# Kernel optimization log

Measured on AMD Instinct MI355X. Metric: run time of the kernel, lower is better.

The kernel has to match this reference:

```python
import jax, jax.numpy as jnp
import numpy as np

B, S, D = 2, 2048, 1024
H = 16
HD = D // H  # 64

def setup_inputs() -> dict:
    key = jax.random.key(0)
    ks = jax.random.split(key, 6)
    s = 1.0 / np.sqrt(D)
    return {
        "x": jax.random.normal(ks[0], (B, S, D), dtype=jnp.float32),
        "Wq": jax.random.normal(ks[1], (D, D), dtype=jnp.float32) * s,
        "Wk": jax.random.normal(ks[2], (D, D), dtype=jnp.float32) * s,
        "Wv": jax.random.normal(ks[3], (D, D), dtype=jnp.float32) * s,
        "Wo": jax.random.normal(ks[4], (D, D), dtype=jnp.float32) * s,
        "bo": jax.random.normal(ks[5], (D,), dtype=jnp.float32) * 0.01,
    }

def reference(x, Wq, Wk, Wv, Wo, bo):
    b, n, _ = x.shape
    # qkv projections (nn.Linear: x @ W^T, no bias for qkv)
    q = (x @ Wq.T).reshape(b, n, H, HD).transpose(0, 2, 1, 3)  # [B,H,S,hd]
    k = (x @ Wk.T).reshape(b, n, H, HD).transpose(0, 2, 1, 3)
    v = (x @ Wv.T).reshape(b, n, H, HD).transpose(0, 2, 1, 3)
    scores = jnp.einsum('bhqd,bhkd->bhqk', q, k)  # [B,H,S,S]
    causal = jnp.triu(jnp.ones((n, n), dtype=bool), k=1)
    scores = jnp.where(causal, -jnp.inf, scores)
    attn = jax.nn.softmax(scores / np.sqrt(HD), axis=-1)
    ctx = jnp.einsum('bhqk,bhkd->bhqd', attn, v)  # [B,H,S,hd]
    ctx = ctx.transpose(0, 2, 1, 3).reshape(b, n, D)
    return ctx @ Wo.T + bo
```

## Files before the change

kernel.cpp:

```cpp
#include <hip/hip_runtime.h>
#include <hip/hip_bf16.h>

typedef __hip_bfloat16 bf16;
typedef short v8s __attribute__((ext_vector_type(8)));
typedef float v4f __attribute__((ext_vector_type(4)));

#define S_ 2048
#define D_ 1024
#define H_ 16
#define HD_ 64

#define EXP2F(x) __builtin_amdgcn_exp2f(x)
#define NEG_BIG (-1.0e30f)
#define C2 0.1803368801111244f

#define GLDS16(g, l) __builtin_amdgcn_global_load_lds(                        \
    (const __attribute__((address_space(1))) unsigned int*)(g),               \
    (__attribute__((address_space(3))) unsigned int*)(l), 16, 0, 0)

static __device__ __forceinline__ unsigned short bf16_bits(bf16 h) {
    union { bf16 h; unsigned short u; } c; c.h = h; return c.u;
}

static __device__ __forceinline__ v8s pack_bf16x8(const float4 a, const float4 b) {
    union { v8s v; unsigned short u[8]; } r;
    r.u[0] = bf16_bits(__float2bfloat16(a.x));
    r.u[1] = bf16_bits(__float2bfloat16(a.y));
    r.u[2] = bf16_bits(__float2bfloat16(a.z));
    r.u[3] = bf16_bits(__float2bfloat16(a.w));
    r.u[4] = bf16_bits(__float2bfloat16(b.x));
    r.u[5] = bf16_bits(__float2bfloat16(b.y));
    r.u[6] = bf16_bits(__float2bfloat16(b.z));
    r.u[7] = bf16_bits(__float2bfloat16(b.w));
    return r.v;
}

__global__ __launch_bounds__(256)
void cvt_bf16(const float* __restrict__ x,  const float* __restrict__ wq,
              const float* __restrict__ wk, const float* __restrict__ wv,
              const float* __restrict__ wo,
              bf16* __restrict__ xb,  bf16* __restrict__ wqb,
              bf16* __restrict__ wkb, bf16* __restrict__ wvb,
              bf16* __restrict__ wob)
{
    const int seg = blockIdx.y;
    const float* src; bf16* dst; int n;
    switch (seg) {
        case 0: src = x;  dst = xb;  n = 4096 * 1024; break;
        case 1: src = wq; dst = wqb; n = 1024 * 1024; break;
        case 2: src = wk; dst = wkb; n = 1024 * 1024; break;
        case 3: src = wv; dst = wvb; n = 1024 * 1024; break;
        default:src = wo; dst = wob; n = 1024 * 1024; break;
    }
    const int idx = (blockIdx.x * 256 + threadIdx.x) * 8;
    if (idx >= n) return;
    *(v8s*)&dst[idx] = pack_bf16x8(*(const float4*)&src[idx],
                                   *(const float4*)&src[idx + 4]);
}

__global__ __launch_bounds__(256)
void gemm_qkv_f(const bf16* __restrict__ xb, const bf16* __restrict__ wqb,
                const bf16* __restrict__ wkb, const bf16* __restrict__ wvb,
                bf16* __restrict__ qd, bf16* __restrict__ kd, bf16* __restrict__ vtd)
{
    const int mode = blockIdx.z;
    const bf16* __restrict__ W = (mode == 0) ? wqb : (mode == 1) ? wkb : wvb;
    const int m0 = blockIdx.x * 128;
    const int n0 = blockIdx.y * 128;
    __shared__ bf16 As[128 * 32];
    __shared__ bf16 Bs[128 * 32];
    const int t    = threadIdx.x;
    const int lane = t & 63, w = t >> 6;
    const int wr = w >> 1, wc = w & 1;
    const int l15 = lane & 15, quad = lane >> 4;
    const int r16 = lane >> 2, c8 = (lane & 3) * 8;
    v4f acc[4][4] = {};

    const bf16* ga = &xb[(m0 + w*16 + r16) * 1024 + c8];
    const bf16* gb = &W [(n0 + w*16 + r16) * 1024 + c8];
    bf16* la0 = &As[w * 16 * 32];
    bf16* la1 = &As[(64 + w * 16) * 32];
    bf16* lb0 = &Bs[w * 16 * 32];
    bf16* lb1 = &Bs[(64 + w * 16) * 32];

    for (int k0 = 0; k0 < 1024; k0 += 32) {
        __syncthreads();
        GLDS16(ga + k0,             la0);
        GLDS16(ga + k0 + 64 * 1024, la1);
        GLDS16(gb + k0,             lb0);
        GLDS16(gb + k0 + 64 * 1024, lb1);
        __syncthreads();
        v8s a[4], b[4];
#pragma unroll
        for (int mt = 0; mt < 4; mt++) a[mt] = *(const v8s*)&As[(wr*64 + mt*16 + l15)*32 + quad*8];
#pragma unroll
        for (int nt = 0; nt < 4; nt++) b[nt] = *(const v8s*)&Bs[(wc*64 + nt*16 + l15)*32 + quad*8];
#pragma unroll
        for (int mt = 0; mt < 4; mt++)
#pragma unroll
            for (int nt = 0; nt < 4; nt++)
                acc[mt][nt] = __builtin_amdgcn_mfma_f32_16x16x32_bf16(a[mt], b[nt], acc[mt][nt], 0, 0, 0);
    }

    const float qscale = (mode == 0) ? C2 : 1.0f;
#pragma unroll
    for (int mt = 0; mt < 4; mt++) {
        const int mb = m0 + wr*64 + mt*16 + quad*4;
        const int b_ = mb >> 11, s = mb & 2047;
#pragma unroll
        for (int nt = 0; nt < 4; nt++) {
            const int n = n0 + wc*64 + nt*16 + l15;
            const int h = n >> 6, d = n & 63;
            if (mode == 2) {
                unsigned int lo = (unsigned int)bf16_bits(__float2bfloat16(acc[mt][nt][0]))
                                | ((unsigned int)bf16_bits(__float2bfloat16(acc[mt][nt][1])) << 16);
                unsigned int hi = (unsigned int)bf16_bits(__float2bfloat16(acc[mt][nt][2]))
                                | ((unsigned int)bf16_bits(__float2bfloat16(acc[mt][nt][3])) << 16);
                uint2 pv; pv.x = lo; pv.y = hi;
                *(uint2*)&vtd[((b_*H_ + h)*HD_ + d)*S_ + s] = pv;
            } else {
                bf16* __restrict__ dst = (mode == 0) ? qd : kd;
#pragma unroll
                for (int r = 0; r < 4; r++)
                    dst[((b_*H_ + h)*S_ + (s + r))*HD_ + d] = __float2bfloat16(acc[mt][nt][r] * qscale);
            }
        }
    }
}

__global__ __launch_bounds__(256)
void gemm_out_f(const bf16* __restrict__ ctx, const bf16* __restrict__ wob,
                const float* __restrict__ bo, float* __restrict__ out)
{
    const int m0 = blockIdx.x * 128;
    const int n0 = blockIdx.y * 128;
    __shared__ bf16 As[128 * 32];
    __shared__ bf16 Bs[128 * 32];
    const int t    = threadIdx.x;
    const int lane = t & 63, w = t >> 6;
    const int wr = w >> 1, wc = w & 1;
    const int l15 = lane & 15, quad = lane >> 4;
    const int r16 = lane >> 2, c8 = (lane & 3) * 8;
    v4f acc[4][4] = {};

    const bf16* ga = &ctx[(m0 + w*16 + r16) * 1024 + c8];
    const bf16* gb = &wob[(n0 + w*16 + r16) * 1024 + c8];
    bf16* la0 = &As[w * 16 * 32];
    bf16* la1 = &As[(64 + w * 16) * 32];
    bf16* lb0 = &Bs[w * 16 * 32];
    bf16* lb1 = &Bs[(64 + w * 16) * 32];

    for (int k0 = 0; k0 < 1024; k0 += 32) {
        __syncthreads();
        GLDS16(ga + k0,             la0);
        GLDS16(ga + k0 + 64 * 1024, la1);
        GLDS16(gb + k0,             lb0);
        GLDS16(gb + k0 + 64 * 1024, lb1);
        __syncthreads();
        v8s a[4], b[4];
#pragma unroll
        for (int mt = 0; mt < 4; mt++) a[mt] = *(const v8s*)&As[(wr*64 + mt*16 + l15)*32 + quad*8];
#pragma unroll
        for (int nt = 0; nt < 4; nt++) b[nt] = *(const v8s*)&Bs[(wc*64 + nt*16 + l15)*32 + quad*8];
#pragma unroll
        for (int mt = 0; mt < 4; mt++)
#pragma unroll
            for (int nt = 0; nt < 4; nt++)
                acc[mt][nt] = __builtin_amdgcn_mfma_f32_16x16x32_bf16(a[mt], b[nt], acc[mt][nt], 0, 0, 0);
    }

#pragma unroll
    for (int mt = 0; mt < 4; mt++) {
        const int mb = m0 + wr*64 + mt*16 + quad*4;
#pragma unroll
        for (int nt = 0; nt < 4; nt++) {
            const int n = n0 + wc*64 + nt*16 + l15;
            const float bias = bo[n];
#pragma unroll
            for (int r = 0; r < 4; r++)
                out[(mb + r)*1024 + n] = acc[mt][nt][r] + bias;
        }
    }
}

__global__ __launch_bounds__(256)
void gemm_qkv(const float* __restrict__ x, const float* __restrict__ Wq,
              const float* __restrict__ Wk, const float* __restrict__ Wv,
              bf16* __restrict__ qd, bf16* __restrict__ kd, bf16* __restrict__ vtd)
{
    const int mode = blockIdx.z;
    const float* __restrict__ W = (mode == 0) ? Wq : (mode == 1) ? Wk : Wv;
    const int m0 = blockIdx.x * 128;
    const int n0 = blockIdx.y * 128;
    __shared__ bf16 As[128 * 40];
    __shared__ bf16 Bs[128 * 40];
    const int t    = threadIdx.x;
    const int lane = t & 63, w = t >> 6;
    const int wr = w >> 1, wc = w & 1;
    const int l15 = lane & 15, quad = lane >> 4;
    const int srow = t >> 2, scol = (t & 3) * 8;
    v4f acc[4][4] = {};

    for (int k0 = 0; k0 < 1024; k0 += 32) {
        __syncthreads();
        {
            const float* pa = &x[(m0 + srow) * 1024 + k0 + scol];
            *(v8s*)&As[srow*40 + scol] = pack_bf16x8(*(const float4*)pa, *(const float4*)(pa + 4));
            const float* pa2 = pa + 64 * 1024;
            *(v8s*)&As[(srow+64)*40 + scol] = pack_bf16x8(*(const float4*)pa2, *(const float4*)(pa2 + 4));
            const float* pb = &W[(n0 + srow) * 1024 + k0 + scol];
            *(v8s*)&Bs[srow*40 + scol] = pack_bf16x8(*(const float4*)pb, *(const float4*)(pb + 4));
            const float* pb2 = pb + 64 * 1024;
            *(v8s*)&Bs[(srow+64)*40 + scol] = pack_bf16x8(*(const float4*)pb2, *(const float4*)(pb2 + 4));
        }
        __syncthreads();
        v8s a[4], b[4];
#pragma unroll
        for (int mt = 0; mt < 4; mt++) a[mt] = *(const v8s*)&As[(wr*64 + mt*16 + l15)*40 + quad*8];
#pragma unroll
        for (int nt = 0; nt < 4; nt++) b[nt] = *(const v8s*)&Bs[(wc*64 + nt*16 + l15)*40 + quad*8];
#pragma unroll
        for (int mt = 0; mt < 4; mt++)
#pragma unroll
            for (int nt = 0; nt < 4; nt++)
                acc[mt][nt] = __builtin_amdgcn_mfma_f32_16x16x32_bf16(a[mt], b[nt], acc[mt][nt], 0, 0, 0);
    }

    const float qscale = (mode == 0) ? C2 : 1.0f;
#pragma unroll
    for (int mt = 0; mt < 4; mt++) {
        const int mb = m0 + wr*64 + mt*16 + quad*4;
        const int b_ = mb >> 11, s = mb & 2047;
#pragma unroll
        for (int nt = 0; nt < 4; nt++) {
            const int n = n0 + wc*64 + nt*16 + l15;
            const int h = n >> 6, d = n & 63;
            if (mode == 2) {
                unsigned int lo = (unsigned int)bf16_bits(__float2bfloat16(acc[mt][nt][0]))
                                | ((unsigned int)bf16_bits(__float2bfloat16(acc[mt][nt][1])) << 16);
                unsigned int hi = (unsigned int)bf16_bits(__float2bfloat16(acc[mt][nt][2]))
                                | ((unsigned int)bf16_bits(__float2bfloat16(acc[mt][nt][3])) << 16);
                uint2 pv; pv.x = lo; pv.y = hi;
                *(uint2*)&vtd[((b_*H_ + h)*HD_ + d)*S_ + s] = pv;
            } else {
                bf16* __restrict__ dst = (mode == 0) ? qd : kd;
#pragma unroll
                for (int r = 0; r < 4; r++)
                    dst[((b_*H_ + h)*S_ + (s + r))*HD_ + d] = __float2bfloat16(acc[mt][nt][r] * qscale);
            }
        }
    }
}

__global__ __launch_bounds__(256)
void gemm_out(const bf16* __restrict__ ctx, const float* __restrict__ Wo,
              const float* __restrict__ bo, float* __restrict__ out)
{
    const int m0 = blockIdx.x * 128;
    const int n0 = blockIdx.y * 128;
    __shared__ bf16 As[128 * 40];
    __shared__ bf16 Bs[128 * 40];
    const int t    = threadIdx.x;
    const int lane = t & 63, w = t >> 6;
    const int wr = w >> 1, wc = w & 1;
    const int l15 = lane & 15, quad = lane >> 4;
    const int srow = t >> 2, scol = (t & 3) * 8;
    v4f acc[4][4] = {};

    for (int k0 = 0; k0 < 1024; k0 += 32) {
        __syncthreads();
        {
            *(v8s*)&As[srow*40 + scol]      = *(const v8s*)&ctx[(m0+srow)*1024 + k0 + scol];
            *(v8s*)&As[(srow+64)*40 + scol] = *(const v8s*)&ctx[(m0+srow+64)*1024 + k0 + scol];
            const float* pb = &Wo[(n0 + srow) * 1024 + k0 + scol];
            *(v8s*)&Bs[srow*40 + scol] = pack_bf16x8(*(const float4*)pb, *(const float4*)(pb + 4));
            const float* pb2 = pb + 64 * 1024;
            *(v8s*)&Bs[(srow+64)*40 + scol] = pack_bf16x8(*(const float4*)pb2, *(const float4*)(pb2 + 4));
        }
        __syncthreads();
        v8s a[4], b[4];
#pragma unroll
        for (int mt = 0; mt < 4; mt++) a[mt] = *(const v8s*)&As[(wr*64 + mt*16 + l15)*40 + quad*8];
#pragma unroll
        for (int nt = 0; nt < 4; nt++) b[nt] = *(const v8s*)&Bs[(wc*64 + nt*16 + l15)*40 + quad*8];
#pragma unroll
        for (int mt = 0; mt < 4; mt++)
#pragma unroll
            for (int nt = 0; nt < 4; nt++)
                acc[mt][nt] = __builtin_amdgcn_mfma_f32_16x16x32_bf16(a[mt], b[nt], acc[mt][nt], 0, 0, 0);
    }

#pragma unroll
    for (int mt = 0; mt < 4; mt++) {
        const int mb = m0 + wr*64 + mt*16 + quad*4;
#pragma unroll
        for (int nt = 0; nt < 4; nt++) {
            const int n = n0 + wc*64 + nt*16 + l15;
            const float bias = bo[n];
#pragma unroll
            for (int r = 0; r < 4; r++)
                out[(mb + r)*1024 + n] = acc[mt][nt][r] + bias;
        }
    }
}

__global__ __launch_bounds__(256)
void flash_attn(const bf16* __restrict__ qd, const bf16* __restrict__ kd,
                const bf16* __restrict__ vtd, bf16* __restrict__ ctx)
{
    const int bh = blockIdx.x;
    const int qb = 15 - blockIdx.y;
    const int t = threadIdx.x;
    const int lane = t & 63, w = t >> 6;
    const int l15 = lane & 15, quad = lane >> 4;
    const int q0 = qb * 128;
    const int nT = 2 * qb + 2;

    __shared__ bf16 Ks[2][64 * 72];
    __shared__ bf16 Vs[2][64 * 72];
    __shared__ bf16 Pl[4][16 * 72];

    const int mrow0 = q0 + w * 16;
    const int mrow1 = q0 + 64 + w * 16;

    v8s qf[2][2];
#pragma unroll
    for (int mt = 0; mt < 2; mt++) {
        const bf16* qb_ = qd + (bh*S_ + (mt ? mrow1 : mrow0) + l15) * HD_;
        qf[mt][0] = *(const v8s*)(qb_ + quad*8);
        qf[mt][1] = *(const v8s*)(qb_ + 32 + quad*8);
    }

    v4f o[2][4] = {};
    float ps[2][4] = {};

    const int rowlo = t >> 3, col8 = (t & 7) * 8;
    const bf16* kp = kd  + (bh*S_ + rowlo)*HD_ + col8;
    const bf16* vp = vtd + (bh*HD_ + rowlo)*S_ + col8;

    v8s pk0 = *(const v8s*)(kp);
    v8s pk1 = *(const v8s*)(kp + 32*HD_);
    v8s pv0 = *(const v8s*)(vp);
    v8s pv1 = *(const v8s*)(vp + 32*S_);

    for (int it = 0; it < nT; ++it) {
        const int c0 = it * 64;
        bf16* Kb = &Ks[it & 1][0];
        bf16* Vb = &Vs[it & 1][0];
        *(v8s*)&Kb[rowlo*72 + col8]      = pk0;
        *(v8s*)&Kb[(rowlo+32)*72 + col8] = pk1;
        *(v8s*)&Vb[rowlo*72 + col8]      = pv0;
        *(v8s*)&Vb[(rowlo+32)*72 + col8] = pv1;
        __syncthreads();
        kp += 64 * HD_;
        vp += 64;
        pk0 = *(const v8s*)(kp);
        pk1 = *(const v8s*)(kp + 32*HD_);
        pv0 = *(const v8s*)(vp);
        pv1 = *(const v8s*)(vp + 32*S_);

        if (c0 <= mrow1 + 15) {
            v8s kf[4][2];
#pragma unroll
            for (int kt = 0; kt < 4; kt++) {
                kf[kt][0] = *(const v8s*)&Kb[(kt*16 + l15)*72 + quad*8];
                kf[kt][1] = *(const v8s*)&Kb[(kt*16 + l15)*72 + 32 + quad*8];
            }
            v8s vf[4][2];
#pragma unroll
            for (int dt = 0; dt < 4; dt++) {
                vf[dt][0] = *(const v8s*)&Vb[(dt*16 + l15)*72 + quad*8];
                vf[dt][1] = *(const v8s*)&Vb[(dt*16 + l15)*72 + 32 + quad*8];
            }

#pragma unroll
            for (int mt = 0; mt < 2; mt++) {
                const int mr = mt ? mrow1 : mrow0;
                if (c0 > mr + 15) continue;
                v4f sc[4] = {};
#pragma unroll
                for (int kt = 0; kt < 4; kt++) {
                    sc[kt] = __builtin_amdgcn_mfma_f32_16x16x32_bf16(qf[mt][0], kf[kt][0], sc[kt], 0, 0, 0);
                    sc[kt] = __builtin_amdgcn_mfma_f32_16x16x32_bf16(qf[mt][1], kf[kt][1], sc[kt], 0, 0, 0);
                }
                const bool full = (c0 + 63 <= mr);
#pragma unroll
                for (int r = 0; r < 4; r++) {
                    const int qg = mr + quad*4 + r;
#pragma unroll
                    for (int kt = 0; kt < 4; kt++) {
                        float s = sc[kt][r];
                        if (!full) {
                            const int kg = c0 + kt*16 + l15;
                            s = (kg <= qg) ? s : NEG_BIG;
                        }
                        const float p = EXP2F(s);
                        sc[kt][r] = p;
                        ps[mt][r] += p;
                    }
                }
                bf16* pw = &Pl[w][0];
#pragma unroll
                for (int kt = 0; kt < 4; kt++)
#pragma unroll
                    for (int r = 0; r < 4; r++)
                        pw[(quad*4 + r)*72 + kt*16 + l15] = __float2bfloat16(sc[kt][r]);
                v8s pf0 = *(const v8s*)&pw[l15*72 + quad*8];
                v8s pf1 = *(const v8s*)&pw[l15*72 + 32 + quad*8];
#pragma unroll
                for (int dt = 0; dt < 4; dt++) {
                    o[mt][dt] = __builtin_amdgcn_mfma_f32_16x16x32_bf16(pf0, vf[dt][0], o[mt][dt], 0, 0, 0);
                    o[mt][dt] = __builtin_amdgcn_mfma_f32_16x16x32_bf16(pf1, vf[dt][1], o[mt][dt], 0, 0, 0);
                }
            }
        }
    }

    const int b_ = bh >> 4, h = bh & 15;
#pragma unroll
    for (int mt = 0; mt < 2; mt++) {
        const int mr = mt ? mrow1 : mrow0;
#pragma unroll
        for (int r = 0; r < 4; r++) {
            float l = ps[mt][r];
#pragma unroll
            for (int off = 1; off < 16; off <<= 1) l += __shfl_xor(l, off);
            const float linv = 1.0f / l;
            const int qg = mr + quad*4 + r;
#pragma unroll
            for (int dt = 0; dt < 4; dt++)
                ctx[(b_*S_ + qg)*D_ + h*HD_ + dt*16 + l15] = __float2bfloat16(o[mt][dt][r] * linv);
        }
    }
}

extern "C" void kernel_launch(void* const* d_in, const int* in_sizes, int n_in,
                              void* d_out, int out_size, void* d_ws, size_t ws_size,
                              hipStream_t stream) {
    const float* x  = (const float*)d_in[0];
    const float* Wq = (const float*)d_in[1];
    const float* Wk = (const float*)d_in[2];
    const float* Wv = (const float*)d_in[3];
    const float* Wo = (const float*)d_in[4];
    const float* bo = (const float*)d_in[5];
    float* out = (float*)d_out;

    const size_t SEG = (size_t)2 * H_ * S_ * HD_;
    bf16* qd  = (bf16*)d_ws;
    bf16* kd  = qd  + SEG;
    bf16* vtd = kd  + SEG;
    bf16* xc  = vtd + SEG;
    bf16* wqb = xc + SEG;
    bf16* wkb = wqb + 1024 * 1024;
    bf16* wvb = wkb + 1024 * 1024;
    bf16* wvv = wvb;
    bf16* wob = wvb + 1024 * 1024;
    (void)wvv;

    const size_t need_fast = (4 * SEG + 4 * 1024 * 1024) * sizeof(bf16);

    if (ws_size >= need_fast) {
        cvt_bf16<<<dim3(2048, 5), 256, 0, stream>>>(x, Wq, Wk, Wv, Wo,
                                                    xc, wqb, wkb, wvb, wob);
        gemm_qkv_f<<<dim3(32, 8, 3), 256, 0, stream>>>(xc, wqb, wkb, wvb, qd, kd, vtd);
        flash_attn<<<dim3(32, 16), 256, 0, stream>>>(qd, kd, vtd, xc);
        gemm_out_f<<<dim3(32, 8), 256, 0, stream>>>(xc, wob, bo, out);
    } else {
        gemm_qkv<<<dim3(32, 8, 3), 256, 0, stream>>>(x, Wq, Wk, Wv, qd, kd, vtd);
        flash_attn<<<dim3(32, 16), 256, 0, stream>>>(qd, kd, vtd, xc);
        gemm_out<<<dim3(32, 8), 256, 0, stream>>>(xc, Wo, bo, out);
    }
}
```

Baseline: 209.3 us.

## Pair causal query blocks per workgroup and load K fragments directly from global

Flash attention now launches 512-thread workgroups that each handle a mirrored pair of query blocks (p and 15-p), so every workgroup does the same amount of causal work and the grid is halved. K tiles are no longer staged through LDS. Each wave loads its K MFMA fragments straight from global memory and prefetches the next tile in registers. Only V still goes through double-buffered LDS, now filled with one 16-byte load per thread. The goal is to remove causal load imbalance and LDS traffic for K, at the cost of redundant K global loads across waves and higher register pressure.

After: 208.4 us. No clear change (-0.4%).

```diff
diff --git a/kernel.cpp b/kernel.cpp
--- a/kernel.cpp
+++ b/kernel.cpp
@@ -304,24 +304,24 @@
     }
 }
 
-__global__ __launch_bounds__(256)
+__global__ __launch_bounds__(512)
 void flash_attn(const bf16* __restrict__ qd, const bf16* __restrict__ kd,
                 const bf16* __restrict__ vtd, bf16* __restrict__ ctx)
 {
     const int bh = blockIdx.x;
-    const int qb = 15 - blockIdx.y;
+    const int p  = blockIdx.y;
     const int t = threadIdx.x;
     const int lane = t & 63, w = t >> 6;
     const int l15 = lane & 15, quad = lane >> 4;
-    const int q0 = qb * 128;
-    const int nT = 2 * qb + 2;
-
-    __shared__ bf16 Ks[2][64 * 72];
+    const int side = w >> 2, wl = w & 3;
+    const int q0 = (side ? (15 - p) : p) * 128;
+    const int nT = 32 - 2 * p;
+
     __shared__ bf16 Vs[2][64 * 72];
-    __shared__ bf16 Pl[4][16 * 72];
-
-    const int mrow0 = q0 + w * 16;
-    const int mrow1 = q0 + 64 + w * 16;
+    __shared__ bf16 Pl[8][16 * 72];
+
+    const int mrow0 = q0 + wl * 16;
+    const int mrow1 = q0 + 64 + wl * 16;
 
     v8s qf[2][2];
 #pragma unroll
@@ -335,37 +335,39 @@
     float ps[2][4] = {};
 
     const int rowlo = t >> 3, col8 = (t & 7) * 8;
-    const bf16* kp = kd  + (bh*S_ + rowlo)*HD_ + col8;
     const bf16* vp = vtd + (bh*HD_ + rowlo)*S_ + col8;
-
-    v8s pk0 = *(const v8s*)(kp);
-    v8s pk1 = *(const v8s*)(kp + 32*HD_);
-    v8s pv0 = *(const v8s*)(vp);
-    v8s pv1 = *(const v8s*)(vp + 32*S_);
+    v8s pv = *(const v8s*)vp;
+
+    const bf16* kbase = kd + (size_t)bh * S_ * HD_;
+    v8s kf[4][2];
+#pragma unroll
+    for (int kt = 0; kt < 4; kt++) {
+        const bf16* kp_ = kbase + (kt*16 + l15)*HD_ + quad*8;
+        kf[kt][0] = *(const v8s*)kp_;
+        kf[kt][1] = *(const v8s*)(kp_ + 32);
+    }
 
     for (int it = 0; it < nT; ++it) {
         const int c0 = it * 64;
-        bf16* Kb = &Ks[it & 1][0];
         bf16* Vb = &Vs[it & 1][0];
-        *(v8s*)&Kb[rowlo*72 + col8]      = pk0;
-        *(v8s*)&Kb[(rowlo+32)*72 + col8] = pk1;
-        *(v8s*)&Vb[rowlo*72 + col8]      = pv0;
-        *(v8s*)&Vb[(rowlo+32)*72 + col8] = pv1;
-        __syncthreads();
-        kp += 64 * HD_;
+        *(v8s*)&Vb[rowlo*72 + col8] = pv;
+        __syncthreads();
         vp += 64;
-        pk0 = *(const v8s*)(kp);
-        pk1 = *(const v8s*)(kp + 32*HD_);
-        pv0 = *(const v8s*)(vp);
-        pv1 = *(const v8s*)(vp + 32*S_);
-
-        if (c0 <= mrow1 + 15) {
-            v8s kf[4][2];
+        pv = *(const v8s*)vp;
+
+        const bool act  = (c0      <= mrow1 + 15);
+        const bool nact = (c0 + 64 <= mrow1 + 15);
+        v8s nkf[4][2];
+        if (nact) {
 #pragma unroll
             for (int kt = 0; kt < 4; kt++) {
-                kf[kt][0] = *(const v8s*)&Kb[(kt*16 + l15)*72 + quad*8];
-                kf[kt][1] = *(const v8s*)&Kb[(kt*16 + l15)*72 + 32 + quad*8];
+                const bf16* kp_ = kbase + (c0 + 64 + kt*16 + l15)*HD_ + quad*8;
+                nkf[kt][0] = *(const v8s*)kp_;
+                nkf[kt][1] = *(const v8s*)(kp_ + 32);
             }
+        }
+
+        if (act) {
             v8s vf[4][2];
 #pragma unroll
             for (int dt = 0; dt < 4; dt++) {
@@ -394,9 +396,9 @@
                             const int kg = c0 + kt*16 + l15;
                             s = (kg <= qg) ? s : NEG_BIG;
                         }
-                        const float p = EXP2F(s);
-                        sc[kt][r] = p;
-                        ps[mt][r] += p;
+                        const float pp = EXP2F(s);
+                        sc[kt][r] = pp;
+                        ps[mt][r] += pp;
                     }
                 }
                 bf16* pw = &Pl[w][0];
@@ -413,6 +415,10 @@
                     o[mt][dt] = __builtin_amdgcn_mfma_f32_16x16x32_bf16(pf1, vf[dt][1], o[mt][dt], 0, 0, 0);
                 }
             }
+        }
+        if (nact) {
+#pragma unroll
+            for (int kt = 0; kt < 4; kt++) { kf[kt][0] = nkf[kt][0]; kf[kt][1] = nkf[kt][1]; }
         }
     }
 
@@ -453,9 +459,7 @@
     bf16* wqb = xc + SEG;
     bf16* wkb = wqb + 1024 * 1024;
     bf16* wvb = wkb + 1024 * 1024;
-    bf16* wvv = wvb;
     bf16* wob = wvb + 1024 * 1024;
-    (void)wvv;
 
     const size_t need_fast = (4 * SEG + 4 * 1024 * 1024) * sizeof(bf16);
 
@@ -463,11 +467,11 @@
         cvt_bf16<<<dim3(2048, 5), 256, 0, stream>>>(x, Wq, Wk, Wv, Wo,
                                                     xc, wqb, wkb, wvb, wob);
         gemm_qkv_f<<<dim3(32, 8, 3), 256, 0, stream>>>(xc, wqb, wkb, wvb, qd, kd, vtd);
-        flash_attn<<<dim3(32, 16), 256, 0, stream>>>(qd, kd, vtd, xc);
+        flash_attn<<<dim3(32, 8), 512, 0, stream>>>(qd, kd, vtd, xc);
         gemm_out_f<<<dim3(32, 8), 256, 0, stream>>>(xc, wob, bo, out);
     } else {
         gemm_qkv<<<dim3(32, 8, 3), 256, 0, stream>>>(x, Wq, Wk, Wv, qd, kd, vtd);
-        flash_attn<<<dim3(32, 16), 256, 0, stream>>>(qd, kd, vtd, xc);
+        flash_attn<<<dim3(32, 8), 512, 0, stream>>>(qd, kd, vtd, xc);
         gemm_out<<<dim3(32, 8), 256, 0, stream>>>(xc, Wo, bo, out);
     }
 }
```

## Restructure flash attention: 64-row tiles, K from registers, shuffle-built P operand

Applied to the files above, without the earlier changes.

Each attention block now covers 64 query rows (one 16-row tile per wave), and the grid doubles to 32x32 blocks. K fragments are loaded straight from global memory into registers and prefetched one tile ahead, so the K shared-memory buffer and its staging go away. Scores are computed transposed (K·Q). The softmax probabilities are packed with v_cvt_pk_bf16_f32 and rearranged into the MFMA A operand through cross-lane shuffles instead of a round trip through shared memory. V moves to an XOR-swizzled 64-wide LDS layout; the trade-offs are more blocks and more per-block K global loads in exchange for less LDS traffic and finer causal load balance.

After: 223.0 us. 1.07x slower.

```diff
diff --git a/kernel.cpp b/kernel.cpp
--- a/kernel.cpp
+++ b/kernel.cpp
@@ -17,6 +17,9 @@
 #define GLDS16(g, l) __builtin_amdgcn_global_load_lds(                        \
     (const __attribute__((address_space(1))) unsigned int*)(g),               \
     (__attribute__((address_space(3))) unsigned int*)(l), 16, 0, 0)
+
+#define CVT_PK(d, lo, hi) \
+    asm("v_cvt_pk_bf16_f32 %0, %1, %2" : "=v"(d) : "v"(lo), "v"(hi))
 
 static __device__ __forceinline__ unsigned short bf16_bits(bf16 h) {
     union { bf16 h; unsigned short u; } c; c.h = h; return c.u;
@@ -309,128 +312,146 @@
                 const bf16* __restrict__ vtd, bf16* __restrict__ ctx)
 {
     const int bh = blockIdx.x;
-    const int qb = 15 - blockIdx.y;
+    const int s  = 31 - (int)blockIdx.y;
     const int t = threadIdx.x;
     const int lane = t & 63, w = t >> 6;
     const int l15 = lane & 15, quad = lane >> 4;
-    const int q0 = qb * 128;
-    const int nT = 2 * qb + 2;
-
-    __shared__ bf16 Ks[2][64 * 72];
-    __shared__ bf16 Vs[2][64 * 72];
-    __shared__ bf16 Pl[4][16 * 72];
-
-    const int mrow0 = q0 + w * 16;
-    const int mrow1 = q0 + 64 + w * 16;
-
-    v8s qf[2][2];
-#pragma unroll
-    for (int mt = 0; mt < 2; mt++) {
-        const bf16* qb_ = qd + (bh*S_ + (mt ? mrow1 : mrow0) + l15) * HD_;
-        qf[mt][0] = *(const v8s*)(qb_ + quad*8);
-        qf[mt][1] = *(const v8s*)(qb_ + 32 + quad*8);
-    }
-
-    v4f o[2][4] = {};
-    float ps[2][4] = {};
-
-    const int rowlo = t >> 3, col8 = (t & 7) * 8;
-    const bf16* kp = kd  + (bh*S_ + rowlo)*HD_ + col8;
-    const bf16* vp = vtd + (bh*HD_ + rowlo)*S_ + col8;
-
-    v8s pk0 = *(const v8s*)(kp);
-    v8s pk1 = *(const v8s*)(kp + 32*HD_);
-    v8s pv0 = *(const v8s*)(vp);
-    v8s pv1 = *(const v8s*)(vp + 32*S_);
+    const int q0 = s * 64 + w * 16;
+    const int nT = s + 1;
+
+    __shared__ bf16 Vs[2][64 * 64];
+
+    const bf16* qp = qd + ((size_t)bh * S_ + q0 + l15) * HD_ + quad * 8;
+    const v8s qf0 = *(const v8s*)qp;
+    const v8s qf1 = *(const v8s*)(qp + 32);
+
+    v4f o[4] = {};
+    float ps = 0.0f;
+
+    const int vrow = t >> 2, vc = (t & 3) * 16;
+    const int wsw = (vrow & 7) << 3;
+    const int vidx0 = (vrow * 64 + vc) ^ wsw;
+    const int vidx1 = (vrow * 64 + vc + 8) ^ wsw;
+    const bf16* vp = vtd + ((size_t)bh * HD_ + vrow) * S_ + vc;
+    v8s pv0 = *(const v8s*)vp;
+    v8s pv1 = *(const v8s*)(vp + 8);
+
+    const bf16* kq = kd + ((size_t)bh * S_ + l15) * HD_ + quad * 8;
+    v8s kf[4][2];
+#pragma unroll
+    for (int kt = 0; kt < 4; kt++) {
+        kf[kt][0] = *(const v8s*)(kq + (kt * 16) * HD_);
+        kf[kt][1] = *(const v8s*)(kq + (kt * 16) * HD_ + 32);
+    }
+
+    const int rsw = (l15 & 7) << 3;
 
     for (int it = 0; it < nT; ++it) {
         const int c0 = it * 64;
-        bf16* Kb = &Ks[it & 1][0];
         bf16* Vb = &Vs[it & 1][0];
-        *(v8s*)&Kb[rowlo*72 + col8]      = pk0;
-        *(v8s*)&Kb[(rowlo+32)*72 + col8] = pk1;
-        *(v8s*)&Vb[rowlo*72 + col8]      = pv0;
-        *(v8s*)&Vb[(rowlo+32)*72 + col8] = pv1;
-        __syncthreads();
-        kp += 64 * HD_;
+        *(v8s*)&Vb[vidx0] = pv0;
+        *(v8s*)&Vb[vidx1] = pv1;
+        __syncthreads();
         vp += 64;
-        pk0 = *(const v8s*)(kp);
-        pk1 = *(const v8s*)(kp + 32*HD_);
-        pv0 = *(const v8s*)(vp);
-        pv1 = *(const v8s*)(vp + 32*S_);
-
-        if (c0 <= mrow1 + 15) {
-            v8s kf[4][2];
+        pv0 = *(const v8s*)vp;
+        pv1 = *(const v8s*)(vp + 8);
+
+        v8s vf[4][2];
+#pragma unroll
+        for (int dt = 0; dt < 4; dt++) {
+            const int rowd = dt * 16 + l15;
+            vf[dt][0] = *(const v8s*)&Vb[(rowd * 64 + quad * 8) ^ rsw];
+            vf[dt][1] = *(const v8s*)&Vb[(rowd * 64 + 32 + quad * 8) ^ rsw];
+        }
+
+        v4f sc[4];
+#pragma unroll
+        for (int kt = 0; kt < 4; kt++) {
+            v4f z = {};
+            z      = __builtin_amdgcn_mfma_f32_16x16x32_bf16(kf[kt][0], qf0, z, 0, 0, 0);
+            sc[kt] = __builtin_amdgcn_mfma_f32_16x16x32_bf16(kf[kt][1], qf1, sc[kt] = z, 0, 0, 0);
+        }
+
+        if (it + 1 < nT) {
+            const bf16* kn = kq + (size_t)(c0 + 64) * HD_;
 #pragma unroll
             for (int kt = 0; kt < 4; kt++) {
-                kf[kt][0] = *(const v8s*)&Kb[(kt*16 + l15)*72 + quad*8];
-                kf[kt][1] = *(const v8s*)&Kb[(kt*16 + l15)*72 + 32 + quad*8];
+                kf[kt][0] = *(const v8s*)(kn + (kt * 16) * HD_);
+                kf[kt][1] = *(const v8s*)(kn + (kt * 16) * HD_ + 32);
             }
-            v8s vf[4][2];
-#pragma unroll
-            for (int dt = 0; dt < 4; dt++) {
-                vf[dt][0] = *(const v8s*)&Vb[(dt*16 + l15)*72 + quad*8];
-                vf[dt][1] = *(const v8s*)&Vb[(dt*16 + l15)*72 + 32 + quad*8];
-            }
-
-#pragma unroll
-            for (int mt = 0; mt < 2; mt++) {
-                const int mr = mt ? mrow1 : mrow0;
-                if (c0 > mr + 15) continue;
-                v4f sc[4] = {};
-#pragma unroll
-                for (int kt = 0; kt < 4; kt++) {
-                    sc[kt] = __builtin_amdgcn_mfma_f32_16x16x32_bf16(qf[mt][0], kf[kt][0], sc[kt], 0, 0, 0);
-                    sc[kt] = __builtin_amdgcn_mfma_f32_16x16x32_bf16(qf[mt][1], kf[kt][1], sc[kt], 0, 0, 0);
+        }
+
+        if (c0 + 63 <= q0) {
+#pragma unroll
+            for (int kt = 0; kt < 4; kt++)
+#pragma unroll
+                for (int r = 0; r < 4; r++) {
+                    const float p = EXP2F(sc[kt][r]);
+                    sc[kt][r] = p; ps += p;
                 }
-                const bool full = (c0 + 63 <= mr);
+        } else {
+            const int kb = c0 - q0 - l15 + quad * 4;
+#pragma unroll
+            for (int kt = 0; kt < 4; kt++)
 #pragma unroll
                 for (int r = 0; r < 4; r++) {
-                    const int qg = mr + quad*4 + r;
-#pragma unroll
-                    for (int kt = 0; kt < 4; kt++) {
-                        float s = sc[kt][r];
-                        if (!full) {
-                            const int kg = c0 + kt*16 + l15;
-                            s = (kg <= qg) ? s : NEG_BIG;
-                        }
-                        const float p = EXP2F(s);
-                        sc[kt][r] = p;
-                        ps[mt][r] += p;
-                    }
+                    const float sv = (kb + kt * 16 + r <= 0) ? sc[kt][r] : NEG_BIG;
+                    const float p = EXP2F(sv);
+                    sc[kt][r] = p; ps += p;
                 }
-                bf16* pw = &Pl[w][0];
-#pragma unroll
-                for (int kt = 0; kt < 4; kt++)
-#pragma unroll
-                    for (int r = 0; r < 4; r++)
-                        pw[(quad*4 + r)*72 + kt*16 + l15] = __float2bfloat16(sc[kt][r]);
-                v8s pf0 = *(const v8s*)&pw[l15*72 + quad*8];
-                v8s pf1 = *(const v8s*)&pw[l15*72 + 32 + quad*8];
-#pragma unroll
-                for (int dt = 0; dt < 4; dt++) {
-                    o[mt][dt] = __builtin_amdgcn_mfma_f32_16x16x32_bf16(pf0, vf[dt][0], o[mt][dt], 0, 0, 0);
-                    o[mt][dt] = __builtin_amdgcn_mfma_f32_16x16x32_bf16(pf1, vf[dt][1], o[mt][dt], 0, 0, 0);
-                }
-            }
-        }
-    }
-
+        }
+
+        unsigned W[4][2];
+#pragma unroll
+        for (int kt = 0; kt < 4; kt++) {
+            CVT_PK(W[kt][0], sc[kt][0], sc[kt][1]);
+            CVT_PK(W[kt][1], sc[kt][2], sc[kt][3]);
+        }
+        const bool qhi = quad >= 2;
+        unsigned X0 = qhi ? W[0][0] : W[1][0];
+        unsigned X1 = qhi ? W[0][1] : W[1][1];
+        unsigned X2 = qhi ? W[2][0] : W[3][0];
+        unsigned X3 = qhi ? W[2][1] : W[3][1];
+        const unsigned A0 = __shfl_xor(X0, 32);
+        const unsigned A1 = __shfl_xor(X1, 32);
+        const unsigned A2 = __shfl_xor(X2, 32);
+        const unsigned A3 = __shfl_xor(X3, 32);
+        unsigned Z0 = (quad == 1) ? W[0][0] : (quad == 2) ? W[1][0] : A0;
+        unsigned Z1 = (quad == 1) ? W[0][1] : (quad == 2) ? W[1][1] : A1;
+        unsigned Z2 = (quad == 1) ? W[2][0] : (quad == 2) ? W[3][0] : A2;
+        unsigned Z3 = (quad == 1) ? W[2][1] : (quad == 2) ? W[3][1] : A3;
+        const unsigned B0 = __shfl_xor(Z0, 16);
+        const unsigned B1 = __shfl_xor(Z1, 16);
+        const unsigned B2 = __shfl_xor(Z2, 16);
+        const unsigned B3 = __shfl_xor(Z3, 16);
+        union { v8s v; unsigned u[4]; } P0, P1;
+        P0.u[0] = (quad == 0) ? W[0][0] : (quad == 2) ? A0 : B0;
+        P0.u[1] = (quad == 0) ? W[0][1] : (quad == 2) ? A1 : B1;
+        P0.u[2] = (quad == 3) ? W[1][0] : (quad == 1) ? A0 : B0;
+        P0.u[3] = (quad == 3) ? W[1][1] : (quad == 1) ? A1 : B1;
+        P1.u[0] = (quad == 0) ? W[2][0] : (quad == 2) ? A2 : B2;
+        P1.u[1] = (quad == 0) ? W[2][1] : (quad == 2) ? A3 : B3;
+        P1.u[2] = (quad == 3) ? W[3][0] : (quad == 1) ? A2 : B2;
+        P1.u[3] = (quad == 3) ? W[3][1] : (quad == 1) ? A3 : B3;
+
+#pragma unroll
+        for (int dt = 0; dt < 4; dt++) {
+            o[dt] = __builtin_amdgcn_mfma_f32_16x16x32_bf16(P0.v, vf[dt][0], o[dt], 0, 0, 0);
+            o[dt] = __builtin_amdgcn_mfma_f32_16x16x32_bf16(P1.v, vf[dt][1], o[dt], 0, 0, 0);
+        }
+    }
+
+    float dsum = ps + __shfl_xor(ps, 16);
+    dsum += __shfl_xor(dsum, 32);
     const int b_ = bh >> 4, h = bh & 15;
 #pragma unroll
-    for (int mt = 0; mt < 2; mt++) {
-        const int mr = mt ? mrow1 : mrow0;
-#pragma unroll
-        for (int r = 0; r < 4; r++) {
-            float l = ps[mt][r];
-#pragma unroll
-            for (int off = 1; off < 16; off <<= 1) l += __shfl_xor(l, off);
-            const float linv = 1.0f / l;
-            const int qg = mr + quad*4 + r;
-#pragma unroll
-            for (int dt = 0; dt < 4; dt++)
-                ctx[(b_*S_ + qg)*D_ + h*HD_ + dt*16 + l15] = __float2bfloat16(o[mt][dt][r] * linv);
-        }
+    for (int r = 0; r < 4; r++) {
+        const float linv = 1.0f / __shfl(dsum, quad * 4 + r);
+        const int qg = q0 + quad * 4 + r;
+#pragma unroll
+        for (int dt = 0; dt < 4; dt++)
+            ctx[((size_t)b_ * S_ + qg) * D_ + h * HD_ + dt * 16 + l15] =
+                __float2bfloat16(o[dt][r] * linv);
     }
 }
 
@@ -453,9 +474,7 @@
     bf16* wqb = xc + SEG;
     bf16* wkb = wqb + 1024 * 1024;
     bf16* wvb = wkb + 1024 * 1024;
-    bf16* wvv = wvb;
     bf16* wob = wvb + 1024 * 1024;
-    (void)wvv;
 
     const size_t need_fast = (4 * SEG + 4 * 1024 * 1024) * sizeof(bf16);
 
@@ -463,11 +482,11 @@
         cvt_bf16<<<dim3(2048, 5), 256, 0, stream>>>(x, Wq, Wk, Wv, Wo,
                                                     xc, wqb, wkb, wvb, wob);
         gemm_qkv_f<<<dim3(32, 8, 3), 256, 0, stream>>>(xc, wqb, wkb, wvb, qd, kd, vtd);
-        flash_attn<<<dim3(32, 16), 256, 0, stream>>>(qd, kd, vtd, xc);
+        flash_attn<<<dim3(32, 32), 256, 0, stream>>>(qd, kd, vtd, xc);
         gemm_out_f<<<dim3(32, 8), 256, 0, stream>>>(xc, wob, bo, out);
     } else {
         gemm_qkv<<<dim3(32, 8, 3), 256, 0, stream>>>(x, Wq, Wk, Wv, qd, kd, vtd);
-        flash_attn<<<dim3(32, 16), 256, 0, stream>>>(qd, kd, vtd, xc);
+        flash_attn<<<dim3(32, 32), 256, 0, stream>>>(qd, kd, vtd, xc);
         gemm_out<<<dim3(32, 8), 256, 0, stream>>>(xc, Wo, bo, out);
     }
 }
```

## Rewrite flash attention as single-wave blocks using 32x32 MFMA and register-resident softmax

Applied to the files above, without the earlier changes.

The attention kernel now runs one 64-lane wave per 32-query block and uses 32x32x16 bf16 MFMAs. K and V^T fragments load straight from global memory into registers, with K prefetched one tile ahead, so the LDS staging and block barriers are gone. P moves from the score accumulator layout to the PV operand layout through packed bf16 converts and permlane32 swaps instead of an LDS round trip. This removes shared-memory traffic and synchronisation, but each wave reloads K/V from global or L2 with no reuse across waves, and the grid grows to 2048 small blocks.

Result: slower. 222.3 us (+6.2%).

```diff
diff --git a/kernel.cpp b/kernel.cpp
--- a/kernel.cpp
+++ b/kernel.cpp
@@ -4,6 +4,7 @@
 typedef __hip_bfloat16 bf16;
 typedef short v8s __attribute__((ext_vector_type(8)));
 typedef float v4f __attribute__((ext_vector_type(4)));
+typedef float v16f __attribute__((ext_vector_type(16)));
 
 #define S_ 2048
 #define D_ 1024
@@ -17,6 +18,14 @@
 #define GLDS16(g, l) __builtin_amdgcn_global_load_lds(                        \
     (const __attribute__((address_space(1))) unsigned int*)(g),               \
     (__attribute__((address_space(3))) unsigned int*)(l), 16, 0, 0)
+
+#define CVT_PK(d, lo, hi) \
+    asm("v_cvt_pk_bf16_f32 %0, %1, %2" : "=v"(d) : "v"(lo), "v"(hi))
+
+#define SWAPHALF(a, b) \
+    asm("v_permlane32_swap_b32 %0, %1" : "+v"(a), "+v"(b))
+
+#define MFMA32(a, b, c) __builtin_amdgcn_mfma_f32_32x32x16_bf16(a, b, c, 0, 0, 0)
 
 static __device__ __forceinline__ unsigned short bf16_bits(bf16 h) {
     union { bf16 h; unsigned short u; } c; c.h = h; return c.u;
@@ -304,133 +313,132 @@
     }
 }
 
-__global__ __launch_bounds__(256)
+#define SOFTMAX_PV(sa, ks0, vA0, vA1, vB0, vB1)                                \
+    {                                                                          \
+        const bool full_ = ((ks0) + 31 <= q0);                                 \
+        if (full_) {                                                           \
+            _Pragma("unroll")                                                  \
+            for (int r = 0; r < 16; r++) {                                     \
+                const float p = EXP2F(sa[r]); sa[r] = p;                       \
+                if (r & 1) ps1 += p; else ps0 += p;                            \
+            }                                                                  \
+        } else {                                                               \
+            const int kb_ = (ks0) + 4 * hi - q0 - l31;                         \
+            _Pragma("unroll")                                                  \
+            for (int r = 0; r < 16; r++) {                                     \
+                const int kl_ = (r & 3) + 8 * (r >> 2);                        \
+                const float p = EXP2F((kb_ + kl_ <= 0) ? sa[r] : NEG_BIG);     \
+                sa[r] = p;                                                     \
+                if (r & 1) ps1 += p; else ps0 += p;                            \
+            }                                                                  \
+        }                                                                      \
+        unsigned u0, u1, u2, u3, u4, u5, u6, u7;                               \
+        CVT_PK(u0, sa[0],  sa[1]);  CVT_PK(u1, sa[2],  sa[3]);                 \
+        CVT_PK(u2, sa[4],  sa[5]);  CVT_PK(u3, sa[6],  sa[7]);                 \
+        CVT_PK(u4, sa[8],  sa[9]);  CVT_PK(u5, sa[10], sa[11]);                \
+        CVT_PK(u6, sa[12], sa[13]); CVT_PK(u7, sa[14], sa[15]);                \
+        SWAPHALF(u0, u2); SWAPHALF(u1, u3);                                    \
+        SWAPHALF(u4, u6); SWAPHALF(u5, u7);                                    \
+        union { v8s v; unsigned w[4]; } pa0_, pa1_;                            \
+        pa0_.w[0] = u0; pa0_.w[1] = u1; pa0_.w[2] = u2; pa0_.w[3] = u3;        \
+        pa1_.w[0] = u4; pa1_.w[1] = u5; pa1_.w[2] = u6; pa1_.w[3] = u7;        \
+        __builtin_amdgcn_s_setprio(1);                                         \
+        o0 = MFMA32(pa0_.v, vA0, o0);                                          \
+        o1 = MFMA32(pa0_.v, vB0, o1);                                          \
+        o0 = MFMA32(pa1_.v, vA1, o0);                                          \
+        o1 = MFMA32(pa1_.v, vB1, o1);                                          \
+        __builtin_amdgcn_s_setprio(0);                                         \
+    }
+
+__global__ __launch_bounds__(64)
 void flash_attn(const bf16* __restrict__ qd, const bf16* __restrict__ kd,
                 const bf16* __restrict__ vtd, bf16* __restrict__ ctx)
 {
     const int bh = blockIdx.x;
-    const int qb = 15 - blockIdx.y;
-    const int t = threadIdx.x;
-    const int lane = t & 63, w = t >> 6;
-    const int l15 = lane & 15, quad = lane >> 4;
-    const int q0 = qb * 128;
-    const int nT = 2 * qb + 2;
-
-    __shared__ bf16 Ks[2][64 * 72];
-    __shared__ bf16 Vs[2][64 * 72];
-    __shared__ bf16 Pl[4][16 * 72];
-
-    const int mrow0 = q0 + w * 16;
-    const int mrow1 = q0 + 64 + w * 16;
-
-    v8s qf[2][2];
-#pragma unroll
-    for (int mt = 0; mt < 2; mt++) {
-        const bf16* qb_ = qd + (bh*S_ + (mt ? mrow1 : mrow0) + l15) * HD_;
-        qf[mt][0] = *(const v8s*)(qb_ + quad*8);
-        qf[mt][1] = *(const v8s*)(qb_ + 32 + quad*8);
-    }
-
-    v4f o[2][4] = {};
-    float ps[2][4] = {};
-
-    const int rowlo = t >> 3, col8 = (t & 7) * 8;
-    const bf16* kp = kd  + (bh*S_ + rowlo)*HD_ + col8;
-    const bf16* vp = vtd + (bh*HD_ + rowlo)*S_ + col8;
-
-    v8s pk0 = *(const v8s*)(kp);
-    v8s pk1 = *(const v8s*)(kp + 32*HD_);
-    v8s pv0 = *(const v8s*)(vp);
-    v8s pv1 = *(const v8s*)(vp + 32*S_);
+    const int m  = 63 - (int)blockIdx.y;
+    const int lane = threadIdx.x;
+    const int l31 = lane & 31, hi = lane >> 5;
+    const int q0 = m * 32;
+    const int nT = (q0 >> 6) + 1;
+
+    const bf16* qp = qd + ((size_t)bh * S_ + q0 + l31) * HD_ + hi * 8;
+    const v8s qf0 = *(const v8s*)(qp);
+    const v8s qf1 = *(const v8s*)(qp + 16);
+    const v8s qf2 = *(const v8s*)(qp + 32);
+    const v8s qf3 = *(const v8s*)(qp + 48);
+
+    v16f o0 = {}, o1 = {};
+    float ps0 = 0.f, ps1 = 0.f;
+
+    const bf16* kq  = kd  + ((size_t)bh * S_ + l31) * HD_ + hi * 8;
+    const bf16* vb0 = vtd + ((size_t)bh * HD_ + l31) * S_ + hi * 8;
+    const bf16* vb1 = vb0 + (size_t)32 * S_;
+
+    v8s kA0 = *(const v8s*)(kq);
+    v8s kA1 = *(const v8s*)(kq + 16);
+    v8s kA2 = *(const v8s*)(kq + 32);
+    v8s kA3 = *(const v8s*)(kq + 48);
+    v8s kB0 = *(const v8s*)(kq + 32 * HD_);
+    v8s kB1 = *(const v8s*)(kq + 32 * HD_ + 16);
+    v8s kB2 = *(const v8s*)(kq + 32 * HD_ + 32);
+    v8s kB3 = *(const v8s*)(kq + 32 * HD_ + 48);
 
     for (int it = 0; it < nT; ++it) {
         const int c0 = it * 64;
-        bf16* Kb = &Ks[it & 1][0];
-        bf16* Vb = &Vs[it & 1][0];
-        *(v8s*)&Kb[rowlo*72 + col8]      = pk0;
-        *(v8s*)&Kb[(rowlo+32)*72 + col8] = pk1;
-        *(v8s*)&Vb[rowlo*72 + col8]      = pv0;
-        *(v8s*)&Vb[(rowlo+32)*72 + col8] = pv1;
-        __syncthreads();
-        kp += 64 * HD_;
-        vp += 64;
-        pk0 = *(const v8s*)(kp);
-        pk1 = *(const v8s*)(kp + 32*HD_);
-        pv0 = *(const v8s*)(vp);
-        pv1 = *(const v8s*)(vp + 32*S_);
-
-        if (c0 <= mrow1 + 15) {
-            v8s kf[4][2];
-#pragma unroll
-            for (int kt = 0; kt < 4; kt++) {
-                kf[kt][0] = *(const v8s*)&Kb[(kt*16 + l15)*72 + quad*8];
-                kf[kt][1] = *(const v8s*)&Kb[(kt*16 + l15)*72 + 32 + quad*8];
-            }
-            v8s vf[4][2];
-#pragma unroll
-            for (int dt = 0; dt < 4; dt++) {
-                vf[dt][0] = *(const v8s*)&Vb[(dt*16 + l15)*72 + quad*8];
-                vf[dt][1] = *(const v8s*)&Vb[(dt*16 + l15)*72 + 32 + quad*8];
-            }
-
-#pragma unroll
-            for (int mt = 0; mt < 2; mt++) {
-                const int mr = mt ? mrow1 : mrow0;
-                if (c0 > mr + 15) continue;
-                v4f sc[4] = {};
-#pragma unroll
-                for (int kt = 0; kt < 4; kt++) {
-                    sc[kt] = __builtin_amdgcn_mfma_f32_16x16x32_bf16(qf[mt][0], kf[kt][0], sc[kt], 0, 0, 0);
-                    sc[kt] = __builtin_amdgcn_mfma_f32_16x16x32_bf16(qf[mt][1], kf[kt][1], sc[kt], 0, 0, 0);
-                }
-                const bool full = (c0 + 63 <= mr);
-#pragma unroll
-                for (int r = 0; r < 4; r++) {
-                    const int qg = mr + quad*4 + r;
-#pragma unroll
-                    for (int kt = 0; kt < 4; kt++) {
-                        float s = sc[kt][r];
-                        if (!full) {
-                            const int kg = c0 + kt*16 + l15;
-                            s = (kg <= qg) ? s : NEG_BIG;
-                        }
-                        const float p = EXP2F(s);
-                        sc[kt][r] = p;
-                        ps[mt][r] += p;
-                    }
-                }
-                bf16* pw = &Pl[w][0];
-#pragma unroll
-                for (int kt = 0; kt < 4; kt++)
-#pragma unroll
-                    for (int r = 0; r < 4; r++)
-                        pw[(quad*4 + r)*72 + kt*16 + l15] = __float2bfloat16(sc[kt][r]);
-                v8s pf0 = *(const v8s*)&pw[l15*72 + quad*8];
-                v8s pf1 = *(const v8s*)&pw[l15*72 + 32 + quad*8];
-#pragma unroll
-                for (int dt = 0; dt < 4; dt++) {
-                    o[mt][dt] = __builtin_amdgcn_mfma_f32_16x16x32_bf16(pf0, vf[dt][0], o[mt][dt], 0, 0, 0);
-                    o[mt][dt] = __builtin_amdgcn_mfma_f32_16x16x32_bf16(pf1, vf[dt][1], o[mt][dt], 0, 0, 0);
-                }
-            }
-        }
-    }
-
-    const int b_ = bh >> 4, h = bh & 15;
-#pragma unroll
-    for (int mt = 0; mt < 2; mt++) {
-        const int mr = mt ? mrow1 : mrow0;
-#pragma unroll
-        for (int r = 0; r < 4; r++) {
-            float l = ps[mt][r];
-#pragma unroll
-            for (int off = 1; off < 16; off <<= 1) l += __shfl_xor(l, off);
-            const float linv = 1.0f / l;
-            const int qg = mr + quad*4 + r;
-#pragma unroll
-            for (int dt = 0; dt < 4; dt++)
-                ctx[(b_*S_ + qg)*D_ + h*HD_ + dt*16 + l15] = __float2bfloat16(o[mt][dt][r] * linv);
-        }
+        const bool a1 = (c0 + 32 <= q0 + 31);
+
+        const bf16* v0 = vb0 + c0;
+        const bf16* v1 = vb1 + c0;
+        const v8s va00 = *(const v8s*)(v0);
+        const v8s va01 = *(const v8s*)(v0 + 16);
+        const v8s vc00 = *(const v8s*)(v1);
+        const v8s vc01 = *(const v8s*)(v1 + 16);
+        const v8s va10 = *(const v8s*)(v0 + 32);
+        const v8s va11 = *(const v8s*)(v0 + 48);
+        const v8s vc10 = *(const v8s*)(v1 + 32);
+        const v8s vc11 = *(const v8s*)(v1 + 48);
+
+        __builtin_amdgcn_s_setprio(1);
+        v16f sa0 = {};
+        sa0 = MFMA32(kA0, qf0, sa0);
+        sa0 = MFMA32(kA1, qf1, sa0);
+        sa0 = MFMA32(kA2, qf2, sa0);
+        sa0 = MFMA32(kA3, qf3, sa0);
+        v16f sa1 = {};
+        if (a1) {
+            sa1 = MFMA32(kB0, qf0, sa1);
+            sa1 = MFMA32(kB1, qf1, sa1);
+            sa1 = MFMA32(kB2, qf2, sa1);
+            sa1 = MFMA32(kB3, qf3, sa1);
+        }
+        __builtin_amdgcn_s_setprio(0);
+
+        if (it + 1 < nT) {
+            const bf16* kn = kq + (size_t)(c0 + 64) * HD_;
+            kA0 = *(const v8s*)(kn);
+            kA1 = *(const v8s*)(kn + 16);
+            kA2 = *(const v8s*)(kn + 32);
+            kA3 = *(const v8s*)(kn + 48);
+            kB0 = *(const v8s*)(kn + 32 * HD_);
+            kB1 = *(const v8s*)(kn + 32 * HD_ + 16);
+            kB2 = *(const v8s*)(kn + 32 * HD_ + 32);
+            kB3 = *(const v8s*)(kn + 32 * HD_ + 48);
+        }
+
+        SOFTMAX_PV(sa0, c0, va00, va01, vc00, vc01);
+        if (a1) SOFTMAX_PV(sa1, c0 + 32, va10, va11, vc10, vc11);
+    }
+
+    const float ps = ps0 + ps1;
+    const float tot = ps + __shfl_xor(ps, 32);
+    const int b_ = bh >> 4, hh = bh & 15;
+    bf16* cb = ctx + ((size_t)b_ * S_ + q0) * D_ + hh * HD_ + l31;
+#pragma unroll
+    for (int r = 0; r < 16; r++) {
+        const int qr = (r & 3) + 8 * (r >> 2) + 4 * hi;
+        const float linv = 1.0f / __shfl(tot, qr);
+        cb[(size_t)qr * D_]      = __float2bfloat16(o0[r] * linv);
+        cb[(size_t)qr * D_ + 32] = __float2bfloat16(o1[r] * linv);
     }
 }
 
@@ -453,9 +461,7 @@
     bf16* wqb = xc + SEG;
     bf16* wkb = wqb + 1024 * 1024;
     bf16* wvb = wkb + 1024 * 1024;
-    bf16* wvv = wvb;
     bf16* wob = wvb + 1024 * 1024;
-    (void)wvv;
 
     const size_t need_fast = (4 * SEG + 4 * 1024 * 1024) * sizeof(bf16);
 
@@ -463,11 +469,11 @@
         cvt_bf16<<<dim3(2048, 5), 256, 0, stream>>>(x, Wq, Wk, Wv, Wo,
                                                     xc, wqb, wkb, wvb, wob);
         gemm_qkv_f<<<dim3(32, 8, 3), 256, 0, stream>>>(xc, wqb, wkb, wvb, qd, kd, vtd);
-        flash_attn<<<dim3(32, 16), 256, 0, stream>>>(qd, kd, vtd, xc);
+        flash_attn<<<dim3(32, 64), 64, 0, stream>>>(qd, kd, vtd, xc);
         gemm_out_f<<<dim3(32, 8), 256, 0, stream>>>(xc, wob, bo, out);
     } else {
         gemm_qkv<<<dim3(32, 8, 3), 256, 0, stream>>>(x, Wq, Wk, Wv, qd, kd, vtd);
-        flash_attn<<<dim3(32, 16), 256, 0, stream>>>(qd, kd, vtd, xc);
+        flash_attn<<<dim3(32, 64), 64, 0, stream>>>(qd, kd, vtd, xc);
         gemm_out<<<dim3(32, 8), 256, 0, stream>>>(xc, Wo, bo, out);
     }
 }
```
